# Kernel tuning notes

Measured on AMD Instinct MI355X. Metric: run time of the kernel, lower is better.

## Reference

```python
import jax, jax.numpy as jnp
import numpy as np

B, T, DIM = 1, 2048, 1024
NUM_HEADS, HEAD_DIM = 8, 128
ATTN_SCALE = 0.12


def _rms_norm(x):
    # F.rms_norm(x, x.size(-1)) with no weight; eps defaults to machine eps
    eps = jnp.asarray(jnp.finfo(x.dtype).eps, x.dtype)
    return x * jax.lax.rsqrt(jnp.mean(x * x, axis=-1, keepdims=True) + eps)


def _rotary_tables(seq_len, head_dim):
    # (1/1024) ** linspace(0,1,head_dim//4), then pad with head_dim//4 zeros
    freq = (1.0 / 1024.0) ** jnp.linspace(0.0, 1.0, head_dim // 4, dtype=jnp.float32)
    ang = jnp.concatenate([freq, jnp.zeros(head_dim // 4, jnp.float32)])  # [hd/2]
    theta = jnp.arange(seq_len, dtype=jnp.float32)[:, None] * ang[None, :]  # [T, hd/2]
    return jnp.cos(theta), jnp.sin(theta)


def _apply_rotary(x, cos, sin):
    # x: [B, T, H, hd]
    x1, x2 = jnp.split(x.astype(jnp.float32), 2, axis=-1)
    c = cos[None, :, None, :]
    s = sin[None, :, None, :]
    y1 = x1 * c + x2 * s
    y2 = -x1 * s + x2 * c
    return jnp.concatenate([y1, y2], axis=-1).astype(x.dtype)


def setup_inputs() -> dict:
    key = jax.random.key(0)
    ks = jax.random.split(key, 5)
    bound = (3.0 ** 0.5) * 0.5 * DIM ** (-0.5)
    x = jax.random.normal(ks[0], (B, T, DIM), jnp.float32)
    ve = jax.random.normal(ks[1], (B, T, NUM_HEADS * HEAD_DIM), jnp.float32)
    qkv_w = jax.random.uniform(ks[2], (3, NUM_HEADS * HEAD_DIM, DIM), jnp.float32, -bound, bound)
    lambdas = jnp.array([0.5, 0.5], jnp.float32)
    # original zero-inits c_proj; use small random weight so the output is nontrivial
    c_proj_w = jax.random.uniform(ks[3], (DIM, NUM_HEADS * HEAD_DIM), jnp.float32, -bound, bound)
    return {"x": x, "ve": ve, "qkv_w": qkv_w, "lambdas": lambdas, "c_proj_w": c_proj_w}


def reference(x, ve, qkv_w, lambdas, c_proj_w):
    Bx, Tx, D = x.shape
    H, hd = NUM_HEADS, HEAD_DIM
    # fused QKV projection: weight [3*H*hd, D]
    qkv = x @ qkv_w.reshape(3 * H * hd, D).T            # [B, T, 3*H*hd]
    qkv = qkv.reshape(Bx, Tx, 3 * H, hd)
    q, k, v = jnp.split(qkv, 3, axis=-2)                # each [B, T, H, hd]
    q, k = _rms_norm(q), _rms_norm(k)
    cos, sin = _rotary_tables(Tx, hd)
    q, k = _apply_rotary(q, cos, sin), _apply_rotary(k, cos, sin)
    v = lambdas[0] * v + lambdas[1] * ve.reshape(v.shape)
    att = jnp.einsum('bthd,bshd->bhts', q, k) * ATTN_SCALE
    causal = jnp.tril(jnp.ones((Tx, Tx), bool))
    att = jnp.where(causal[None, None], att, -jnp.inf)
    att = jax.nn.softmax(att, axis=-1)
    y = jnp.einsum('bhts,bshd->bthd', att, v).reshape(Bx, Tx, H * hd)
    return y @ c_proj_w.T
```

## Files before the change

### kernel.cpp

```cpp
#include <hip/hip_runtime.h>


typedef __attribute__((ext_vector_type(8))) short short8;
typedef __attribute__((ext_vector_type(4))) short short4b;
typedef __attribute__((ext_vector_type(4))) float fx4;
typedef __attribute__((ext_vector_type(8))) unsigned short ushort8;
typedef __attribute__((ext_vector_type(4))) unsigned short ushort4v;
typedef __attribute__((ext_vector_type(2))) unsigned short ushort2v;
typedef __attribute__((ext_vector_type(4))) float float4v;

#define T_SEQ 2048
#define NH 8
#define HD 128

__device__ __forceinline__ unsigned short f2bf(float f) {
  union { float f; unsigned u; } v; v.f = f;
  unsigned u = v.u;
  u += 0x7fffu + ((u >> 16) & 1u);
  return (unsigned short)(u >> 16);
}
__device__ __forceinline__ short bf_t(float f) {
  union { float f; unsigned u; } v; v.f = f;
  return (short)(v.u >> 16);
}
__device__ __forceinline__ float bf2f(unsigned short h) {
  union { unsigned u; float f; } v; v.u = ((unsigned)h) << 16;
  return v.f;
}

typedef __attribute__((address_space(1))) unsigned int glb_u32;
typedef __attribute__((address_space(3))) unsigned int lds_u32;
__device__ __forceinline__ void gl_lds16(const unsigned short* g, unsigned short* l) {
  __builtin_amdgcn_global_load_lds((const glb_u32*)g, (lds_u32*)l, 16, 0, 0);
}

__global__ __launch_bounds__(256) void cast3_kernel(
    const float* __restrict__ x, const float* __restrict__ w1,
    const float* __restrict__ w2, unsigned short* __restrict__ o) {
  long q = (long)blockIdx.x * 256 + threadIdx.x;
  const float* src;
  if (q < 524288)        src = x  + 4 * q;
  else if (q < 1310720)  src = w1 + 4 * (q - 524288);
  else                   src = w2 + 4 * (q - 1310720);
  float4v v = *(const float4v*)src;
  ushort4v r;
  r[0] = f2bf(v[0]); r[1] = f2bf(v[1]); r[2] = f2bf(v[2]); r[3] = f2bf(v[3]);
  *(ushort4v*)(o + 4 * q) = r;
}

template <bool OUT_BF16, int BM, int BN>
__global__ __launch_bounds__(256, 2) void gemm_bt4(
    const unsigned short* __restrict__ A, const unsigned short* __restrict__ B,
    void* __restrict__ Cp, int M, int N, int K) {
  constexpr int MT = BM / 32;
  constexpr int NT = BN / 32;
  constexpr int ASEG = BM / 8;
  constexpr int NLOAD = (BM + BN) / 32;
  __shared__ unsigned short a_sh[2][BM * 64];
  __shared__ unsigned short b_sh[2][BN * 64];
  const int tid = threadIdx.x;
  const int wave = tid >> 6, lane = tid & 63;
  const int ln = lane & 15, quad = lane >> 4;
  const int wm = wave & 1, wn = wave >> 1;
  const long arow0 = (long)blockIdx.y * BM;
  const long brow0 = (long)blockIdx.x * BN;

  const unsigned short* gsrc[NLOAD];
  unsigned short* ldst[NLOAD];
  int bstr[NLOAD];
  for (int i = 0; i < NLOAD; ++i) {
    int s = wave * NLOAD + i;
    int isB = s >= ASEG;
    int srel = isB ? s - ASEG : s;
    int li = srel * 64 + lane;
    int row = li >> 3, posc = li & 7;
    int c = posc ^ (row & 7);
    gsrc[i] = (isB ? B + brow0 * (long)K : A + arow0 * (long)K)
              + (long)row * K + c * 8;
    ldst[i] = (isB ? &b_sh[0][0] : &a_sh[0][0]) + srel * 512;
    bstr[i] = isB ? BN * 64 : BM * 64;
  }
  for (int i = 0; i < NLOAD; ++i) gl_lds16(gsrc[i], ldst[i]);

  fx4 acc[MT][NT] = {};
  int cur = 0;
  for (int k0 = 0; k0 < K; k0 += 64, cur ^= 1) {
    __syncthreads();
    if (k0 + 64 < K)
      for (int i = 0; i < NLOAD; ++i)
        gl_lds16(gsrc[i] + k0 + 64, ldst[i] + (cur ^ 1) * bstr[i]);
    const unsigned short* ash = &a_sh[cur][0];
    const unsigned short* bsh = &b_sh[cur][0];
    short8 af[2][MT], bfr[2][NT];
    for (int kq = 0; kq < 2; ++kq) {
      for (int mt = 0; mt < MT; ++mt) {
        int m = wm * (BM / 2) + mt * 16 + ln;
        int pos = (kq * 4 + quad) ^ (m & 7);
        af[kq][mt] = *(const short8*)&ash[m * 64 + pos * 8];
      }
      for (int nt = 0; nt < NT; ++nt) {
        int n = wn * (BN / 2) + nt * 16 + ln;
        int pos = (kq * 4 + quad) ^ (n & 7);
        bfr[kq][nt] = *(const short8*)&bsh[n * 64 + pos * 8];
      }
    }
    for (int kq = 0; kq < 2; ++kq)
      for (int mt = 0; mt < MT; ++mt)
        for (int nt = 0; nt < NT; ++nt)
          acc[mt][nt] = __builtin_amdgcn_mfma_f32_16x16x32_bf16(
              af[kq][mt], bfr[kq][nt], acc[mt][nt], 0, 0, 0);
  }
  for (int mt = 0; mt < MT; ++mt)
    for (int nt = 0; nt < NT; ++nt)
      for (int r = 0; r < 4; ++r) {
        long row = arow0 + wm * (BM / 2) + mt * 16 + quad * 4 + r;
        long col = brow0 + wn * (BN / 2) + nt * 16 + ln;
        float v = acc[mt][nt][r];
        if constexpr (OUT_BF16)
          ((unsigned short*)Cp)[row * N + col] = f2bf(v);
        else
          ((float*)Cp)[row * N + col] = v;
      }
}

__global__ __launch_bounds__(256) void prep_qkv(
    const unsigned short* __restrict__ qkv, const float* __restrict__ ve,
    const float* __restrict__ lambdas, unsigned short* __restrict__ qh,
    unsigned short* __restrict__ kh, unsigned short* __restrict__ vt) {
  __shared__ unsigned short lt[64 * 72];
  const int bx = blockIdx.x, h = blockIdx.y;
  const int tid = threadIdx.x;

  if (bx < 128) {
    const int r2 = tid >> 5, c = tid & 31;
    float ang[2];
    for (int u = 0; u < 2; ++u) {
      int dd = 2 * c + u;
      ang[u] = (dd < 32) ? exp2f(-10.0f * (float)dd / 31.0f) : 0.0f;
    }
    for (int rr = 0; rr < 2; ++rr) {
      int t = bx * 16 + rr * 8 + r2;
      float cv[2], sv[2];
      for (int u = 0; u < 2; ++u) {
        float th = (float)t * ang[u];
        sv[u] = __sinf(th); cv[u] = __cosf(th);
      }
      for (int which = 0; which < 2; ++which) {
        const unsigned short* src = qkv + (long)t * 3072 + which * 1024 + h * 128;
        ushort2v aa = *(const ushort2v*)(src + 2 * c);
        ushort2v bb = *(const ushort2v*)(src + 64 + 2 * c);
        float x1[2] = { bf2f(aa[0]), bf2f(aa[1]) };
        float x2[2] = { bf2f(bb[0]), bf2f(bb[1]) };
        float ss = x1[0]*x1[0] + x1[1]*x1[1] + x2[0]*x2[0] + x2[1]*x2[1];
        for (int off = 1; off < 32; off <<= 1) ss += __shfl_xor(ss, off);
        float rn = rsqrtf(ss * (1.0f / 128.0f) + 1.1920929e-7f);
        ushort2v o1, o2;
        for (int u = 0; u < 2; ++u) {
          float y1 = ( x1[u] * cv[u] + x2[u] * sv[u]) * rn;
          float y2 = (-x1[u] * sv[u] + x2[u] * cv[u]) * rn;
          o1[u] = f2bf(y1); o2[u] = f2bf(y2);
        }
        unsigned short* dst = (which ? kh : qh) + ((long)h * T_SEQ + t) * 128;
        *(ushort2v*)(dst + 2 * c) = o1;
        *(ushort2v*)(dst + 64 + 2 * c) = o2;
      }
    }
  } else {
    const int vb = bx - 128;
    const int tt = vb >> 1, dsub = vb & 1;
    const float l0 = lambdas[0], l1 = lambdas[1];
    const int r = tid >> 2, cb = (tid & 3) * 16;
    const unsigned short* vs = qkv + (long)(tt * 64 + r) * 3072 + 2048
                               + h * 128 + dsub * 64 + cb;
    const float* es = ve + (long)(tt * 64 + r) * 1024 + h * 128 + dsub * 64 + cb;
    ushort8 vv[2];
    for (int q = 0; q < 2; ++q) vv[q] = *(const ushort8*)(vs + 8 * q);
    float4v ee[4];
    for (int q = 0; q < 4; ++q) ee[q] = *(const float4v*)(es + 4 * q);
    for (int j = 0; j < 16; ++j) {
      float v = bf2f(vv[j >> 3][j & 7]) * l0 + ee[j >> 2][j & 3] * l1;
      lt[(cb + j) * 72 + r] = f2bf(v);
    }
    __syncthreads();
    const int d = tid >> 2, quarter = tid & 3;
    unsigned short* dst = vt + ((long)h * HD + dsub * 64 + d) * T_SEQ
                          + tt * 64 + quarter * 16;
    const unsigned short* srcl = &lt[d * 72];
    for (int g = 0; g < 4; ++g) {
      int p0 = quarter * 16 + g * 4;
      int kv0 = ((p0 >> 5) & 1) * 32 + ((p0 >> 2) & 1) * 16 + ((p0 >> 3) & 3) * 4;
      *(ushort4v*)(dst + g * 4) = *(const ushort4v*)(srcl + kv0);
    }
  }
}

#define ATT_C1 0.17312340490667562f
#define ATT_C2 23.083120654223415f

__global__ __launch_bounds__(256, 2) void attn_part(
    const unsigned short* __restrict__ qh, const unsigned short* __restrict__ kh,
    const unsigned short* __restrict__ vt, unsigned short* __restrict__ Yp,
    float* __restrict__ lp) {
  __shared__ unsigned short kbuf[2][8192];
  __shared__ unsigned short vbuf[2][8192];
  const int tid = threadIdx.x;
  const int wave = tid >> 6, lane = tid & 63;
  const int ln = lane & 15, quad = lane >> 4;
  const int qt = blockIdx.x, h = blockIdx.y, ch = blockIdx.z;
  const int jmax = 2 * qt + 1;
  const int j0 = ch * 4;
  if (j0 > jmax) return;
  const int j1 = min(j0 + 3, jmax);

  int qg[2];
  short8 qf[2][4];
  for (int s = 0; s < 2; ++s) {
    qg[s] = qt * 128 + wave * 32 + s * 16 + ln;
    const unsigned short* qbase = qh + ((long)h * T_SEQ + qg[s]) * 128;
    for (int kc = 0; kc < 4; ++kc)
      qf[s][kc] = *(const short8*)(qbase + kc * 32 + quad * 8);
  }
  fx4 accy[2][8] = {};
  float l_loc[2] = {0.f, 0.f};

  const unsigned short* kg[4]; unsigned short* kl[4];
  const unsigned short* vg[4]; unsigned short* vl[4];
  for (int i = 0; i < 4; ++i) {
    int s = wave * 4 + i;
    { int li = s * 64 + lane; int row = li >> 4, posc = li & 15;
      int c = posc ^ (row & 15);
      kg[i] = kh + ((long)h * T_SEQ + row) * 128 + c * 8;
      kl[i] = &kbuf[0][s * 512]; }
    { int li = s * 64 + lane; int row = li >> 3, posc = li & 7;
      int c = posc ^ (row & 7);
      vg[i] = vt + ((long)h * HD + row) * T_SEQ + c * 8;
      vl[i] = &vbuf[0][s * 512]; }
  }
  for (int i = 0; i < 4; ++i) gl_lds16(kg[i] + (long)j0 * 8192, kl[i]);
  for (int i = 0; i < 4; ++i) gl_lds16(vg[i] + (long)j0 * 64, vl[i]);

  int cur = 0;
  for (int jt = j0; jt <= j1; ++jt, cur ^= 1) {
    __syncthreads();
    if (jt < j1) {
      int nb = (cur ^ 1) * 8192;
      for (int i = 0; i < 4; ++i) gl_lds16(kg[i] + (long)(jt + 1) * 8192, kl[i] + nb);
      for (int i = 0; i < 4; ++i) gl_lds16(vg[i] + (long)(jt + 1) * 64, vl[i] + nb);
    }
    const unsigned short* kb_ = &kbuf[cur][0];
    fx4 s4[2][4];
    for (int kt = 0; kt < 4; ++kt) {
      s4[0][kt] = fx4{0.f, 0.f, 0.f, 0.f};
      s4[1][kt] = fx4{0.f, 0.f, 0.f, 0.f};
      for (int kc = 0; kc < 4; ++kc) {
        int pos = (kc * 4 + quad) ^ ln;
        short8 kf = *(const short8*)&kb_[(kt * 16 + ln) * 128 + pos * 8];
        s4[0][kt] = __builtin_amdgcn_mfma_f32_16x16x32_bf16(kf, qf[0][kc], s4[0][kt], 0, 0, 0);
        s4[1][kt] = __builtin_amdgcn_mfma_f32_16x16x32_bf16(kf, qf[1][kc], s4[1][kt], 0, 0, 0);
      }
    }
    short4b pb[2][4];
    for (int s = 0; s < 2; ++s)
      for (int kt = 0; kt < 4; ++kt) {
        int kvb = jt * 64 + kt * 16 + quad * 4;
        float p[4];
        for (int r = 0; r < 4; ++r)
          p[r] = exp2f(fmaf(s4[s][kt][r], ATT_C1, -ATT_C2));
        if (jt * 64 + kt * 16 + 15 > qt * 128 + wave * 32 + s * 16) {
          for (int r = 0; r < 4; ++r) if (kvb + r > qg[s]) p[r] = 0.f;
        }
        l_loc[s] += (p[0] + p[1]) + (p[2] + p[3]);
        pb[s][kt] = short4b{ bf_t(p[0]), bf_t(p[1]), bf_t(p[2]), bf_t(p[3]) };
      }
    const unsigned short* vb_ = &vbuf[cur][0];
    for (int kh2 = 0; kh2 < 2; ++kh2) {
      for (int dt = 0; dt < 8; ++dt) {
        int row = dt * 16 + ln;
        int pos = (kh2 * 4 + quad) ^ (ln & 7);
        short8 va = *(const short8*)&vb_[row * 64 + pos * 8];
        short4b va0 = { va[0], va[1], va[2], va[3] };
        short4b va1 = { va[4], va[5], va[6], va[7] };
        for (int s = 0; s < 2; ++s) {
          accy[s][dt] = __builtin_amdgcn_mfma_f32_16x16x16bf16_1k(
              va0, pb[s][kh2 * 2], accy[s][dt], 0, 0, 0);
          accy[s][dt] = __builtin_amdgcn_mfma_f32_16x16x16bf16_1k(
              va1, pb[s][kh2 * 2 + 1], accy[s][dt], 0, 0, 0);
        }
      }
    }
  }

  int cbase = qt + ((qt - 1) * (qt - 1)) / 4;
  const long pp = (long)(h * 72 + cbase + ch);
  for (int s = 0; s < 2; ++s) {
    float l = l_loc[s];
    l += __shfl_xor(l, 16);
    l += __shfl_xor(l, 32);
    int q = wave * 32 + s * 16 + ln;
    if (quad == 0) lp[pp * 128 + q] = l;
    unsigned short* yb = Yp + pp * 16384 + (long)q * 128;
    for (int dt = 0; dt < 8; ++dt) {
      ushort4v o;
      for (int r = 0; r < 4; ++r) o[r] = f2bf(accy[s][dt][r]);
      *(ushort4v*)(yb + dt * 16 + quad * 4) = o;
    }
  }
}

__global__ __launch_bounds__(256) void attn_combine(
    const unsigned short* __restrict__ Yp, const float* __restrict__ lp,
    unsigned short* __restrict__ y) {
  const int bx = blockIdx.x, h = blockIdx.y;
  const int tid = threadIdx.x;
  const int row = bx * 16 + (tid >> 4);
  const int cb  = (tid & 15) * 8;
  const int qt = row >> 7;
  const int r128 = row & 127;
  const int nc = (qt >> 1) + 1;
  const int cbase = qt + ((qt - 1) * (qt - 1)) / 4;
  float acc[8];
  for (int j = 0; j < 8; ++j) acc[j] = 0.f;
  float ltot = 0.f;
  for (int c = 0; c < nc; ++c) {
    long pp = (long)(h * 72 + cbase + c);
    const unsigned short* ys = Yp + pp * 16384 + (long)r128 * 128 + cb;
    ltot += lp[pp * 128 + r128];
    ushort8 v = *(const ushort8*)ys;
    for (int j = 0; j < 8; ++j) acc[j] += bf2f(v[j]);
  }
  float inv = 1.f / ltot;
  unsigned short* dst = y + (long)row * 1024 + h * 128 + cb;
  ushort8 o;
  for (int j = 0; j < 8; ++j) o[j] = f2bf(acc[j] * inv);
  *(ushort8*)dst = o;
}

extern "C" void kernel_launch(void* const* d_in, const int* in_sizes, int n_in,
                              void* d_out, int out_size, void* d_ws, size_t ws_size,
                              hipStream_t stream) {
  const float* x       = (const float*)d_in[0];
  const float* ve      = (const float*)d_in[1];
  const float* qkv_w   = (const float*)d_in[2];
  const float* lambdas = (const float*)d_in[3];
  const float* c_proj  = (const float*)d_in[4];
  char* ws = (char*)d_ws;
  unsigned short* qkv_bf = (unsigned short*)(ws);
  unsigned short* x_bf   = (unsigned short*)(ws + 12582912);
  unsigned short* wqkv   = (unsigned short*)(ws + 16777216);
  unsigned short* wproj  = (unsigned short*)(ws + 23068672);
  unsigned short* qhat   = (unsigned short*)(ws + 25165824);
  unsigned short* khat   = (unsigned short*)(ws + 29360128);
  unsigned short* vtb    = (unsigned short*)(ws + 33554432);
  unsigned short* ybf    = (unsigned short*)(ws + 37748736);
  unsigned short* Yp     = (unsigned short*)(ws);
  float*          lpart  = (float*)(ws + 18874368);
  float* out = (float*)d_out;

  cast3_kernel<<<6144, 256, 0, stream>>>(x, qkv_w, c_proj, x_bf);
  gemm_bt4<true, 128, 128><<<dim3(24, 16), 256, 0, stream>>>(x_bf, wqkv, qkv_bf, 2048, 3072, 1024);
  prep_qkv<<<dim3(192, 8), 256, 0, stream>>>(qkv_bf, ve, lambdas, qhat, khat, vtb);
  attn_part<<<dim3(16, 8, 8), 256, 0, stream>>>(qhat, khat, vtb, Yp, lpart);
  attn_combine<<<dim3(128, 8), 256, 0, stream>>>(Yp, lpart, ybf);
  gemm_bt4<false, 64, 64><<<dim3(16, 32), 256, 0, stream>>>(ybf, wproj, out, 2048, 1024, 1024);
}
```

Baseline: 170.6 us.

## Fuse QKV projection GEMM with rmsnorm, rotary and value-mix epilogue

```diff
diff --git a/kernel.cpp b/kernel.cpp
--- a/kernel.cpp
+++ b/kernel.cpp
@@ -46,6 +46,145 @@
   ushort4v r;
   r[0] = f2bf(v[0]); r[1] = f2bf(v[1]); r[2] = f2bf(v[2]); r[3] = f2bf(v[3]);
   *(ushort4v*)(o + 4 * q) = r;
+}
+
+__global__ __launch_bounds__(256, 2) void gemm_qkv(
+    const unsigned short* __restrict__ A, const unsigned short* __restrict__ B,
+    const float* __restrict__ ve, const float* __restrict__ lambdas,
+    unsigned short* __restrict__ qh, unsigned short* __restrict__ kh,
+    unsigned short* __restrict__ vt) {
+  constexpr int BM = 128, BN = 128, MT = 4, NT = 4;
+  constexpr int ASEG = BM / 8;
+  constexpr int NLOAD = (BM + BN) / 32;
+  constexpr int K = 1024;
+  __shared__ unsigned short smem[32768];
+  unsigned short* a_sh = smem;
+  unsigned short* b_sh = smem + 16384;
+  const int tid = threadIdx.x;
+  const int wave = tid >> 6, lane = tid & 63;
+  const int ln = lane & 15, quad = lane >> 4;
+  const int wm = wave & 1, wn = wave >> 1;
+  const long arow0 = (long)blockIdx.y * BM;
+  const long brow0 = (long)blockIdx.x * BN;
+
+  const unsigned short* gsrc[NLOAD];
+  unsigned short* ldst[NLOAD];
+  for (int i = 0; i < NLOAD; ++i) {
+    int s = wave * NLOAD + i;
+    int isB = s >= ASEG;
+    int srel = isB ? s - ASEG : s;
+    int li = srel * 64 + lane;
+    int row = li >> 3, posc = li & 7;
+    int c = posc ^ (row & 7);
+    gsrc[i] = (isB ? B + brow0 * (long)K : A + arow0 * (long)K)
+              + (long)row * K + c * 8;
+    ldst[i] = (isB ? b_sh : a_sh) + srel * 512;
+  }
+  for (int i = 0; i < NLOAD; ++i) gl_lds16(gsrc[i], ldst[i]);
+
+  fx4 acc[MT][NT] = {};
+  int cur = 0;
+  for (int k0 = 0; k0 < K; k0 += 64, cur ^= 1) {
+    __syncthreads();
+    if (k0 + 64 < K)
+      for (int i = 0; i < NLOAD; ++i)
+        gl_lds16(gsrc[i] + k0 + 64, ldst[i] + (cur ^ 1) * 8192);
+    const unsigned short* ash = a_sh + cur * 8192;
+    const unsigned short* bsh = b_sh + cur * 8192;
+    short8 af[2][MT], bfr[2][NT];
+    for (int kq = 0; kq < 2; ++kq) {
+      for (int mt = 0; mt < MT; ++mt) {
+        int m = wm * 64 + mt * 16 + ln;
+        int pos = (kq * 4 + quad) ^ (m & 7);
+        af[kq][mt] = *(const short8*)&ash[m * 64 + pos * 8];
+      }
+      for (int nt = 0; nt < NT; ++nt) {
+        int n = wn * 64 + nt * 16 + ln;
+        int pos = (kq * 4 + quad) ^ (n & 7);
+        bfr[kq][nt] = *(const short8*)&bsh[n * 64 + pos * 8];
+      }
+    }
+    for (int kq = 0; kq < 2; ++kq)
+      for (int mt = 0; mt < MT; ++mt)
+        for (int nt = 0; nt < NT; ++nt)
+          acc[mt][nt] = __builtin_amdgcn_mfma_f32_16x16x32_bf16(
+              af[kq][mt], bfr[kq][nt], acc[mt][nt], 0, 0, 0);
+  }
+
+  const int which = (int)(blockIdx.x >> 3), h = (int)(blockIdx.x & 7);
+  __syncthreads();
+  unsigned short* lt = smem;
+  for (int mt = 0; mt < MT; ++mt)
+    for (int nt = 0; nt < NT; ++nt)
+      for (int r = 0; r < 4; ++r) {
+        int row = wm * 64 + mt * 16 + quad * 4 + r;
+        int col = wn * 64 + nt * 16 + ln;
+        lt[row * 136 + col] = f2bf(acc[mt][nt][r]);
+      }
+  __syncthreads();
+
+  if (which < 2) {
+    const int r2 = tid >> 5, c = tid & 31;
+    float ang[2];
+    for (int u = 0; u < 2; ++u) {
+      int dd = 2 * c + u;
+      ang[u] = (dd < 32) ? exp2f(-10.0f * (float)dd / 31.0f) : 0.0f;
+    }
+    unsigned short* dstb = (which ? kh : qh) + ((long)h * T_SEQ + arow0) * 128;
+    for (int rr = 0; rr < 16; ++rr) {
+      int tl = rr * 8 + r2;
+      float tg = (float)(arow0 + tl);
+      float cv[2], sv[2];
+      for (int u = 0; u < 2; ++u) {
+        float th = tg * ang[u];
+        sv[u] = __sinf(th); cv[u] = __cosf(th);
+      }
+      ushort2v aa = *(const ushort2v*)&lt[tl * 136 + 2 * c];
+      ushort2v bb = *(const ushort2v*)&lt[tl * 136 + 64 + 2 * c];
+      float x1[2] = { bf2f(aa[0]), bf2f(aa[1]) };
+      float x2[2] = { bf2f(bb[0]), bf2f(bb[1]) };
+      float ss = x1[0]*x1[0] + x1[1]*x1[1] + x2[0]*x2[0] + x2[1]*x2[1];
+      for (int off = 1; off < 32; off <<= 1) ss += __shfl_xor(ss, off);
+      float rn = rsqrtf(ss * (1.0f / 128.0f) + 1.1920929e-7f);
+      ushort2v o1, o2;
+      for (int u = 0; u < 2; ++u) {
+        float y1 = ( x1[u] * cv[u] + x2[u] * sv[u]) * rn;
+        float y2 = (-x1[u] * sv[u] + x2[u] * cv[u]) * rn;
+        o1[u] = f2bf(y1); o2[u] = f2bf(y2);
+      }
+      unsigned short* dst = dstb + (long)tl * 128;
+      *(ushort2v*)(dst + 2 * c) = o1;
+      *(ushort2v*)(dst + 64 + 2 * c) = o2;
+    }
+  } else {
+    unsigned short* lt2 = smem + 17408;
+    const float l0 = lambdas[0], l1 = lambdas[1];
+    for (int sub = 0; sub < 4; ++sub) {
+      const int tt2 = sub >> 1, dsub = sub & 1;
+      const int r = tid >> 2, cb = (tid & 3) * 16;
+      const unsigned short* vrow = &lt[(tt2 * 64 + r) * 136 + dsub * 64 + cb];
+      const float* es = ve + (arow0 + tt2 * 64 + r) * 1024 + h * 128 + dsub * 64 + cb;
+      ushort8 vv[2];
+      for (int q = 0; q < 2; ++q) vv[q] = *(const ushort8*)(vrow + 8 * q);
+      float4v ee[4];
+      for (int q = 0; q < 4; ++q) ee[q] = *(const float4v*)(es + 4 * q);
+      for (int j = 0; j < 16; ++j) {
+        float v = bf2f(vv[j >> 3][j & 7]) * l0 + ee[j >> 2][j & 3] * l1;
+        lt2[(cb + j) * 72 + r] = f2bf(v);
+      }
+      __syncthreads();
+      const int d = tid >> 2, quarter = tid & 3;
+      unsigned short* dst = vt + ((long)h * HD + dsub * 64 + d) * T_SEQ
+                            + arow0 + tt2 * 64 + quarter * 16;
+      const unsigned short* srcl = &lt2[d * 72];
+      for (int g = 0; g < 4; ++g) {
+        int p0 = quarter * 16 + g * 4;
+        int kv0 = ((p0 >> 5) & 1) * 32 + ((p0 >> 2) & 1) * 16 + ((p0 >> 3) & 3) * 4;
+        *(ushort4v*)(dst + g * 4) = *(const ushort4v*)(srcl + kv0);
+      }
+      __syncthreads();
+    }
+  }
 }
 
 template <bool OUT_BF16, int BM, int BN>
@@ -121,77 +260,6 @@
         else
           ((float*)Cp)[row * N + col] = v;
       }
-}
-
-__global__ __launch_bounds__(256) void prep_qkv(
-    const unsigned short* __restrict__ qkv, const float* __restrict__ ve,
-    const float* __restrict__ lambdas, unsigned short* __restrict__ qh,
-    unsigned short* __restrict__ kh, unsigned short* __restrict__ vt) {
-  __shared__ unsigned short lt[64 * 72];
-  const int bx = blockIdx.x, h = blockIdx.y;
-  const int tid = threadIdx.x;
-
-  if (bx < 128) {
-    const int r2 = tid >> 5, c = tid & 31;
-    float ang[2];
-    for (int u = 0; u < 2; ++u) {
-      int dd = 2 * c + u;
-      ang[u] = (dd < 32) ? exp2f(-10.0f * (float)dd / 31.0f) : 0.0f;
-    }
-    for (int rr = 0; rr < 2; ++rr) {
-      int t = bx * 16 + rr * 8 + r2;
-      float cv[2], sv[2];
-      for (int u = 0; u < 2; ++u) {
-        float th = (float)t * ang[u];
-        sv[u] = __sinf(th); cv[u] = __cosf(th);
-      }
-      for (int which = 0; which < 2; ++which) {
-        const unsigned short* src = qkv + (long)t * 3072 + which * 1024 + h * 128;
-        ushort2v aa = *(const ushort2v*)(src + 2 * c);
-        ushort2v bb = *(const ushort2v*)(src + 64 + 2 * c);
-        float x1[2] = { bf2f(aa[0]), bf2f(aa[1]) };
-        float x2[2] = { bf2f(bb[0]), bf2f(bb[1]) };
-        float ss = x1[0]*x1[0] + x1[1]*x1[1] + x2[0]*x2[0] + x2[1]*x2[1];
-        for (int off = 1; off < 32; off <<= 1) ss += __shfl_xor(ss, off);
-        float rn = rsqrtf(ss * (1.0f / 128.0f) + 1.1920929e-7f);
-        ushort2v o1, o2;
-        for (int u = 0; u < 2; ++u) {
-          float y1 = ( x1[u] * cv[u] + x2[u] * sv[u]) * rn;
-          float y2 = (-x1[u] * sv[u] + x2[u] * cv[u]) * rn;
-          o1[u] = f2bf(y1); o2[u] = f2bf(y2);
-        }
-        unsigned short* dst = (which ? kh : qh) + ((long)h * T_SEQ + t) * 128;
-        *(ushort2v*)(dst + 2 * c) = o1;
-        *(ushort2v*)(dst + 64 + 2 * c) = o2;
-      }
-    }
-  } else {
-    const int vb = bx - 128;
-    const int tt = vb >> 1, dsub = vb & 1;
-    const float l0 = lambdas[0], l1 = lambdas[1];
-    const int r = tid >> 2, cb = (tid & 3) * 16;
-    const unsigned short* vs = qkv + (long)(tt * 64 + r) * 3072 + 2048
-                               + h * 128 + dsub * 64 + cb;
-    const float* es = ve + (long)(tt * 64 + r) * 1024 + h * 128 + dsub * 64 + cb;
-    ushort8 vv[2];
-    for (int q = 0; q < 2; ++q) vv[q] = *(const ushort8*)(vs + 8 * q);
-    float4v ee[4];
-    for (int q = 0; q < 4; ++q) ee[q] = *(const float4v*)(es + 4 * q);
-    for (int j = 0; j < 16; ++j) {
-      float v = bf2f(vv[j >> 3][j & 7]) * l0 + ee[j >> 2][j & 3] * l1;
-      lt[(cb + j) * 72 + r] = f2bf(v);
-    }
-    __syncthreads();
-    const int d = tid >> 2, quarter = tid & 3;
-    unsigned short* dst = vt + ((long)h * HD + dsub * 64 + d) * T_SEQ
-                          + tt * 64 + quarter * 16;
-    const unsigned short* srcl = &lt[d * 72];
-    for (int g = 0; g < 4; ++g) {
-      int p0 = quarter * 16 + g * 4;
-      int kv0 = ((p0 >> 5) & 1) * 32 + ((p0 >> 2) & 1) * 16 + ((p0 >> 3) & 3) * 4;
-      *(ushort4v*)(dst + g * 4) = *(const ushort4v*)(srcl + kv0);
-    }
-  }
 }
 
 #define ATT_C1 0.17312340490667562f
@@ -344,7 +412,6 @@
   const float* lambdas = (const float*)d_in[3];
   const float* c_proj  = (const float*)d_in[4];
   char* ws = (char*)d_ws;
-  unsigned short* qkv_bf = (unsigned short*)(ws);
   unsigned short* x_bf   = (unsigned short*)(ws + 12582912);
   unsigned short* wqkv   = (unsigned short*)(ws + 16777216);
   unsigned short* wproj  = (unsigned short*)(ws + 23068672);
@@ -357,8 +424,7 @@
   float* out = (float*)d_out;
 
   cast3_kernel<<<6144, 256, 0, stream>>>(x, qkv_w, c_proj, x_bf);
-  gemm_bt4<true, 128, 128><<<dim3(24, 16), 256, 0, stream>>>(x_bf, wqkv, qkv_bf, 2048, 3072, 1024);
-  prep_qkv<<<dim3(192, 8), 256, 0, stream>>>(qkv_bf, ve, lambdas, qhat, khat, vtb);
+  gemm_qkv<<<dim3(24, 16), 256, 0, stream>>>(x_bf, wqkv, ve, lambdas, qhat, khat, vtb);
   attn_part<<<dim3(16, 8, 8), 256, 0, stream>>>(qhat, khat, vtb, Yp, lpart);
   attn_combine<<<dim3(128, 8), 256, 0, stream>>>(Yp, lpart, ybf);
   gemm_bt4<false, 64, 64><<<dim3(16, 32), 256, 0, stream>>>(ybf, wproj, out, 2048, 1024, 1024);
```

After: 184.2 us. 8.0% more time.
